# Kernel optimization log

Hardware: AMD Instinct MI355X
Metric: run time of the kernel (lower is better)

The kernel has to match this reference:

```python
import jax, jax.numpy as jnp
import numpy as np

CODEBOOK_BITS = 8      # log2(256)
NUM_Q = 2              # NUM_QUANTIZERS
INV_TEMP = 100.0       # LFQ default inv_temperature
DIVERSITY_GAMMA = 1.0
ENTROPY_WEIGHT = 0.1   # LFQ default entropy_loss_weight
COMMIT_WEIGHT = 1.0


def conv2d(x, w, b, pad):
    out = jax.lax.conv_general_dilated(
        x, w, (1, 1), [(pad, pad), (pad, pad)],
        dimension_numbers=('NCHW', 'OIHW', 'NCHW'))
    return out + b[None, :, None, None]


def maxpool2(x):
    return jax.lax.reduce_window(x, -jnp.inf, jax.lax.max,
                                 (1, 1, 2, 2), (1, 1, 2, 2), 'VALID')


def groupnorm(x, groups=4, eps=1e-5):
    B, C, H, W = x.shape
    xg = x.reshape(B, groups, C // groups, H, W)
    mu = xg.mean(axis=(2, 3, 4), keepdims=True)
    var = xg.var(axis=(2, 3, 4), keepdims=True)
    return ((xg - mu) * jax.lax.rsqrt(var + eps)).reshape(B, C, H, W)


def upsample2(x):  # nearest, scale 2
    return jnp.repeat(jnp.repeat(x, 2, axis=2), 2, axis=3)


def lfq_codebook():
    # all 2^8 sign patterns, code j has bit i = ((j>>i)&1)*2-1
    j = jnp.arange(2 ** CODEBOOK_BITS)
    bits = ((j[:, None] >> jnp.arange(CODEBOOK_BITS)[None, :]) & 1).astype(jnp.float32)
    return bits * 2.0 - 1.0  # [256, 8]


def lfq_residual(z):
    # z: (B, D, H, W) with D = CODEBOOK_BITS
    codebook = lfq_codebook()
    t = jnp.transpose(z, (0, 2, 3, 1))  # (B,H,W,D) tokens
    residual = t
    quantized_out = jnp.zeros_like(t)
    pow2 = (2 ** jnp.arange(CODEBOOK_BITS)).astype(jnp.int32)
    indices = []
    aux = jnp.zeros((), t.dtype)
    for _ in range(NUM_Q):
        q_hard = jnp.where(residual > 0, 1.0, -1.0).astype(t.dtype)
        # straight-through binarization
        q = residual + jax.lax.stop_gradient(q_hard - residual)
        idx = jnp.sum((q_hard > 0).astype(jnp.int32) * pow2, axis=-1)  # (B,H,W)
        logits = (2.0 * INV_TEMP) * jnp.einsum('bhwd,cd->bhwc', residual, codebook)
        logp = jax.nn.log_softmax(logits, axis=-1)
        probs = jnp.exp(logp)
        per_sample_entropy = -jnp.mean(jnp.sum(probs * logp, axis=-1))
        avg_prob = jnp.mean(probs.reshape(-1, probs.shape[-1]), axis=0)
        codebook_entropy = -jnp.sum(avg_prob * jnp.log(avg_prob + 1e-10))
        entropy_aux = per_sample_entropy - DIVERSITY_GAMMA * codebook_entropy
        commit = jnp.mean((residual - jax.lax.stop_gradient(q_hard)) ** 2)
        aux = aux + ENTROPY_WEIGHT * entropy_aux + COMMIT_WEIGHT * commit
        quantized_out = quantized_out + q
        residual = residual - jax.lax.stop_gradient(q)
        indices.append(idx)
    q_out = jnp.transpose(quantized_out, (0, 3, 1, 2))  # (B,D,H,W)
    return q_out, jnp.stack(indices, axis=-1), aux


def setup_inputs() -> dict:
    key = jax.random.key(0)
    ks = jax.random.split(key, 13)
    s = 0.05
    return {
        'x': jax.random.normal(ks[0], (32, 1, 256, 256), jnp.float32),
        'w1': jax.random.normal(ks[1], (16, 1, 3, 3), jnp.float32) * s,
        'b1': jax.random.normal(ks[2], (16,), jnp.float32) * s,
        'w2': jax.random.normal(ks[3], (32, 16, 3, 3), jnp.float32) * s,
        'b2': jax.random.normal(ks[4], (32,), jnp.float32) * s,
        'w3': jax.random.normal(ks[5], (8, 32, 1, 1), jnp.float32) * s,
        'b3': jax.random.normal(ks[6], (8,), jnp.float32) * s,
        'd1': jax.random.normal(ks[7], (32, 8, 3, 3), jnp.float32) * s,
        'db1': jax.random.normal(ks[8], (32,), jnp.float32) * s,
        'd2': jax.random.normal(ks[9], (16, 32, 3, 3), jnp.float32) * s,
        'db2': jax.random.normal(ks[10], (16,), jnp.float32) * s,
        'd3': jax.random.normal(ks[11], (1, 16, 3, 3), jnp.float32) * s,
        'db3': jax.random.normal(ks[12], (1,), jnp.float32) * s,
    }


def reference(x, w1, b1, w2, b2, w3, b3, d1, db1, d2, db2, d3, db3):
    # encode
    h = jax.nn.gelu(maxpool2(conv2d(x, w1, b1, pad=1)), approximate=False)
    h = groupnorm(maxpool2(conv2d(h, w2, b2, pad=1)))
    h = conv2d(h, w3, b3, pad=0)  # (B,8,64,64)
    # residual LFQ
    q, indices, aux = lfq_residual(h)
    # decode
    y = upsample2(conv2d(q, d1, db1, pad=1))
    y = upsample2(jax.nn.gelu(conv2d(y, d2, db2, pad=1), approximate=False))
    y = conv2d(y, d3, db3, pad=1)
    return jnp.clip(y, -1.0, 1.0), indices, aux
```

## Files before the change

kernel.cpp:

```cpp
#include <hip/hip_runtime.h>
#include <hip/hip_bf16.h>
#include <math.h>

#define DEV __device__ __forceinline__

DEV float gelu_exact(float x){ return 0.5f*x*(1.0f + erff(x*0.70710678118654752f)); }

__global__ __launch_bounds__(256) void k_prep(const float* __restrict__ w2,
    const float* __restrict__ d2, float* __restrict__ w2t, float* __restrict__ wp4d2)
{
  const int gid = blockIdx.x*256 + threadIdx.x;
  for(int i=gid;i<4608;i+=2048){
    int oc=i/144, rem=i-oc*144, ic=rem/9, k=rem-ic*9;
    w2t[(ic*32+oc)*9+k]=w2[i];
  }
  for(int i=gid;i<2048;i+=2048){
    int par=i>>9, ic=(i>>4)&31, oc=i&15;
    int py=par>>1, px=par&1;
    const float* wg = d2 + ((size_t)oc*32+ic)*9;
    float a00=0.f,a01=0.f,a10=0.f,a11=0.f;
    #pragma unroll
    for(int ky=0;ky<3;ky++){
      int sy = py ? (ky>>1) : ((ky>0)?1:0);
      #pragma unroll
      for(int kx=0;kx<3;kx++){
        int sx = px ? (kx>>1) : ((kx>0)?1:0);
        float wv=wg[ky*3+kx];
        if(sy==0){ if(sx==0)a00+=wv; else a01+=wv; }
        else     { if(sx==0)a10+=wv; else a11+=wv; }
      }
    }
    float* dst=wp4d2+(size_t)i*4;
    dst[0]=a00; dst[1]=a01; dst[2]=a10; dst[3]=a11;
  }
}

__global__ __launch_bounds__(256) void k_conv1(const float* __restrict__ x,
    const float* __restrict__ w1, const float* __restrict__ b1,
    float* __restrict__ h1)
{
  __shared__ float sE[34*19], sO[34*19];
  const int b = blockIdx.z;
  const int r0 = blockIdx.x*32, c0 = blockIdx.y*32;
  const float* xp = x + (size_t)b*65536;
  for(int i=threadIdx.x;i<34*34;i+=256){
    int r=i/34, c=i-r*34;
    int gr=r0+r-1, gc=c0+c-1;
    float v=0.f;
    if(gr>=0 && gr<256 && gc>=0 && gc<256) v = xp[gr*256+gc];
    if(c&1) sO[r*19+(c>>1)]=v; else sE[r*19+(c>>1)]=v;
  }
  __syncthreads();
  const int tx=threadIdx.x&15, ty=threadIdx.x>>4;
  const int base = 2*ty*19 + tx;
  float in[4][4];
  #pragma unroll
  for(int r=0;r<4;r++){
    in[r][0]=sE[base+r*19]; in[r][1]=sO[base+r*19];
    in[r][2]=sE[base+r*19+1]; in[r][3]=sO[base+r*19+1];
  }
  const int py = blockIdx.x*16+ty, px = blockIdx.y*16+tx;
  float* op = h1 + ((size_t)b*16)*16384 + py*128 + px;
  #pragma unroll
  for(int ch=0;ch<16;ch++){
    float m=-1e30f;
    #pragma unroll
    for(int pr=0;pr<2;pr++)
      #pragma unroll
      for(int pc=0;pc<2;pc++){
        float a=0.f;
        #pragma unroll
        for(int ky=0;ky<3;ky++)
          #pragma unroll
          for(int kx=0;kx<3;kx++)
            a = fmaf(in[pr+ky][pc+kx], w1[ch*9+ky*3+kx], a);
        m = fmaxf(m,a);
      }
    op[(size_t)ch*16384] = gelu_exact(m + b1[ch]);
  }
}

__global__ __launch_bounds__(256) void k_conv2(const float* __restrict__ h1,
    const float* __restrict__ w2t, const float* __restrict__ b2,
    float* __restrict__ h2, double* __restrict__ pb)
{
  __shared__ __align__(16) float t2[8*360];
  const int b=blockIdx.z;
  const int r0=blockIdx.x*16, c0=blockIdx.y*16;
  const float* hp = h1 + (size_t)b*16*16384;
  const int pos=threadIdx.x&63;
  const int ocg=__builtin_amdgcn_readfirstlane((int)(threadIdx.x>>6));
  const int oc0=ocg*8;
  const int pyl=pos>>3, pxl=pos&7;
  const int base0 = 2*pyl*20 + 2*pxl;
  float acc[8][4];
  #pragma unroll
  for(int o=0;o<8;o++)
    #pragma unroll
    for(int j=0;j<4;j++) acc[o][j]=0.f;

  for(int half=0;half<2;half++){
    for(int i=threadIdx.x;i<1296;i+=256){
      int ic=i/162, rem=i-ic*162, lr=rem/9, jp=rem-lr*9;
      int gr=r0+lr-1, gc=c0+2*jp-1;
      float v0=0.f, v1=0.f;
      if(gr>=0&&gr<128){
        const float* row=hp+(size_t)(half*8+ic)*16384+(size_t)gr*128;
        if(gc>=0&&gc<128) v0=row[gc];
        if(gc+1<128)      v1=row[gc+1];
      }
      *(float2*)&t2[ic*360+lr*20+2*jp]=make_float2(v0,v1);
    }
    __syncthreads();
    #pragma unroll 4
    for(int ic=0;ic<8;ic++){
      float in[4][4];
      #pragma unroll
      for(int r=0;r<4;r++){
        float2 a=*(const float2*)&t2[ic*360 + base0 + r*20];
        float2 c=*(const float2*)&t2[ic*360 + base0 + r*20 + 2];
        in[r][0]=a.x; in[r][1]=a.y; in[r][2]=c.x; in[r][3]=c.y;
      }
      const float* wp = w2t + ((half*8+ic)*32+oc0)*9;
      #pragma unroll
      for(int o=0;o<8;o++){
        #pragma unroll
        for(int pr=0;pr<2;pr++)
          #pragma unroll
          for(int pc=0;pc<2;pc++){
            float s=acc[o][pr*2+pc];
            #pragma unroll
            for(int ky=0;ky<3;ky++)
              #pragma unroll
              for(int kx=0;kx<3;kx++)
                s=fmaf(in[pr+ky][pc+kx], wp[o*9+ky*3+kx], s);
            acc[o][pr*2+pc]=s;
          }
      }
    }
    __syncthreads();
  }
  const int py=blockIdx.x*8+pyl, px=blockIdx.y*8+pxl;
  double s=0.0, s2=0.0;
  #pragma unroll
  for(int o=0;o<8;o++){
    const int oc=oc0+o;
    float m=fmaxf(fmaxf(acc[o][0],acc[o][1]),fmaxf(acc[o][2],acc[o][3]));
    float hv=m+b2[oc];
    h2[(((size_t)b*32+oc)*64+py)*64+px]=hv;
    s += (double)hv; s2 += (double)hv*(double)hv;
  }
  #pragma unroll
  for(int off=32;off;off>>=1){
    s  += __shfl_xor(s,  off, 64);
    s2 += __shfl_xor(s2, off, 64);
  }
  if(pos==0){
    const int bidx = blockIdx.x*8 + blockIdx.y;
    double* p = pb + (((size_t)b*4+ocg)*64 + bidx)*2;
    p[0]=s; p[1]=s2;
  }
}

__global__ __launch_bounds__(64) void k_stats2(const double* __restrict__ pb,
                                               float* __restrict__ stats)
{
  const int bg=blockIdx.x, t=threadIdx.x;
  double s = pb[((size_t)bg*64+t)*2], s2 = pb[((size_t)bg*64+t)*2+1];
  #pragma unroll
  for(int off=32;off;off>>=1){
    s  += __shfl_xor(s,  off, 64);
    s2 += __shfl_xor(s2, off, 64);
  }
  if(t==0){
    double mu=s/32768.0;
    double var=s2/32768.0 - mu*mu;
    stats[bg]=(float)mu;
    stats[128+bg]=(float)(1.0/sqrt(var+1e-5));
  }
}

__global__ __launch_bounds__(256) void k_lfq(const float* __restrict__ h2,
    const float* __restrict__ stats, const float* __restrict__ w3, const float* __restrict__ b3,
    float* __restrict__ qout, float* __restrict__ idxout,
    float* __restrict__ avgp, float* __restrict__ ec)
{
  __shared__ __align__(16) float tabL[16*258];
  __shared__ __align__(16) float tabH[16*258];
  const int blk=blockIdx.x;
  const int b=blk>>4;
  const int t=threadIdx.x;
  const int h=(blk&15)*4 + (t>>6);
  const int w=t&63;
  float mu[4], rs[4];
  #pragma unroll
  for(int g=0;g<4;g++){ mu[g]=stats[b*4+g]; rs[g]=stats[128+b*4+g]; }
  const float* hp = h2 + (size_t)b*131072 + h*64 + w;
  float z[8];
  #pragma unroll
  for(int d=0;d<8;d++) z[d]=b3[d];
  #pragma unroll
  for(int c=0;c<32;c++){
    float xn=(hp[(size_t)c*4096]-mu[c>>3])*rs[c>>3];
    #pragma unroll
    for(int d=0;d<8;d++) z[d]=fmaf(xn, w3[d*32+c], z[d]);
  }
  float r[8], qsum[8];
  #pragma unroll
  for(int d=0;d<8;d++){ r[d]=z[d]; qsum[d]=0.f; }
  float entk[2], comk[2];
  #pragma unroll
  for(int k=0;k<2;k++){
    int idx=0; float ent=0.f, com=0.f;
    float pb0[8], pb1[8];
    #pragma unroll
    for(int d=0;d<8;d++){
      float rv=r[d];
      bool pos = rv>0.f;
      float sgn = pos?1.f:-1.f;
      idx |= (pos?1:0)<<d;
      float dd=rv-sgn; com=fmaf(dd,dd,com);
      float a=400.f*fabsf(rv);
      float e=__expf(-a);
      float p=1.f/(1.f+e);
      ent += a - p*a - __logf(p);
      float pm=p, pq=1.f-p;
      pb1[d]=pos?pm:pq;
      pb0[d]=pos?pq:pm;
      qsum[d]+=sgn;
      r[d]=rv-sgn;
    }
    float lo[16], hi[16];
    lo[0]=pb0[0]; lo[1]=pb1[0];
    lo[2]=lo[0]*pb1[1]; lo[3]=lo[1]*pb1[1]; lo[0]*=pb0[1]; lo[1]*=pb0[1];
    lo[4]=lo[0]*pb1[2]; lo[5]=lo[1]*pb1[2]; lo[6]=lo[2]*pb1[2]; lo[7]=lo[3]*pb1[2];
    lo[0]*=pb0[2]; lo[1]*=pb0[2]; lo[2]*=pb0[2]; lo[3]*=pb0[2];
    lo[8]=lo[0]*pb1[3]; lo[9]=lo[1]*pb1[3]; lo[10]=lo[2]*pb1[3]; lo[11]=lo[3]*pb1[3];
    lo[12]=lo[4]*pb1[3]; lo[13]=lo[5]*pb1[3]; lo[14]=lo[6]*pb1[3]; lo[15]=lo[7]*pb1[3];
    lo[0]*=pb0[3]; lo[1]*=pb0[3]; lo[2]*=pb0[3]; lo[3]*=pb0[3];
    lo[4]*=pb0[3]; lo[5]*=pb0[3]; lo[6]*=pb0[3]; lo[7]*=pb0[3];
    hi[0]=pb0[4]; hi[1]=pb1[4];
    hi[2]=hi[0]*pb1[5]; hi[3]=hi[1]*pb1[5]; hi[0]*=pb0[5]; hi[1]*=pb0[5];
    hi[4]=hi[0]*pb1[6]; hi[5]=hi[1]*pb1[6]; hi[6]=hi[2]*pb1[6]; hi[7]=hi[3]*pb1[6];
    hi[0]*=pb0[6]; hi[1]*=pb0[6]; hi[2]*=pb0[6]; hi[3]*=pb0[6];
    hi[8]=hi[0]*pb1[7]; hi[9]=hi[1]*pb1[7]; hi[10]=hi[2]*pb1[7]; hi[11]=hi[3]*pb1[7];
    hi[12]=hi[4]*pb1[7]; hi[13]=hi[5]*pb1[7]; hi[14]=hi[6]*pb1[7]; hi[15]=hi[7]*pb1[7];
    hi[0]*=pb0[7]; hi[1]*=pb0[7]; hi[2]*=pb0[7]; hi[3]*=pb0[7];
    hi[4]*=pb0[7]; hi[5]*=pb0[7]; hi[6]*=pb0[7]; hi[7]*=pb0[7];
    #pragma unroll
    for(int m=0;m<16;m++){ tabL[m*258+t]=lo[m]; tabH[m*258+t]=hi[m]; }
    __syncthreads();
    float accp=0.f, accq=0.f;
    const int jl=t&15, jh=t>>4;
    const float* Lp=&tabL[jl*258];
    const float* Hp=&tabH[jh*258];
    #pragma unroll 8
    for(int q=0;q<128;q++){
      float2 L=*(const float2*)&Lp[2*q];
      float2 H=*(const float2*)&Hp[2*q];
      accp=fmaf(L.x,H.x,accp); accq=fmaf(L.y,H.y,accq);
    }
    avgp[((size_t)k*512+blk)*256+t]=accp+accq;
    __syncthreads();
    entk[k]=ent; comk[k]=com;
    idxout[((size_t)(b*64+h)*64+w)*2+k]=(float)idx;
  }
  #pragma unroll
  for(int d=0;d<8;d++)
    qout[(((size_t)b*8+d)*64+h)*64+w]=qsum[d];
  tabL[t]=entk[0]; tabL[256+t]=entk[1]; tabL[512+t]=comk[0]; tabL[768+t]=comk[1];
  __syncthreads();
  for(int st=128;st>0;st>>=1){
    if(t<st){ tabL[t]+=tabL[t+st]; tabL[256+t]+=tabL[256+t+st];
              tabL[512+t]+=tabL[512+t+st]; tabL[768+t]+=tabL[768+t+st]; }
    __syncthreads();
  }
  if(t==0){ ec[blk*4+0]=tabL[0]; ec[blk*4+1]=tabL[256]; ec[blk*4+2]=tabL[512]; ec[blk*4+3]=tabL[768]; }
}

__global__ __launch_bounds__(256) void k_red(const float* __restrict__ avgp,
    float* __restrict__ avgs)
{
  const int k=blockIdx.x>>4, c0=(blockIdx.x&15)*16;
  const int col=threadIdx.x&15, rg=threadIdx.x>>4;
  float s=0.f;
  for(int j=0;j<32;j++){
    int blk=rg+16*j;
    s+=avgp[((size_t)k*512+blk)*256+c0+col];
  }
  __shared__ float red[256];
  red[threadIdx.x]=s; __syncthreads();
  for(int st=128;st>=16;st>>=1){
    if(threadIdx.x<st) red[threadIdx.x]+=red[threadIdx.x+st];
    __syncthreads();
  }
  if(threadIdx.x<16) avgs[k*256+c0+threadIdx.x]=red[threadIdx.x];
}

__global__ __launch_bounds__(256) void k_final(const float* __restrict__ avgs,
    const float* __restrict__ ec, float* __restrict__ auxout)
{
  __shared__ double red[256];
  const int t=threadIdx.x;
  double cb=0.0;
  #pragma unroll
  for(int k=0;k<2;k++){
    double ap=(double)avgs[k*256+t]*(1.0/131072.0);
    cb += -(ap*log(ap+1e-10));
  }
  red[t]=cb; __syncthreads();
  for(int st=128;st>0;st>>=1){ if(t<st) red[t]+=red[t+st]; __syncthreads(); }
  double CB=red[0]; __syncthreads();
  double e=0.0,c=0.0;
  for(int blk=t;blk<512;blk+=256){
    e += (double)ec[blk*4+0]+(double)ec[blk*4+1];
    c += (double)ec[blk*4+2]+(double)ec[blk*4+3];
  }
  red[t]=e; __syncthreads();
  for(int st=128;st>0;st>>=1){ if(t<st) red[t]+=red[t+st]; __syncthreads(); }
  double E=red[0]; __syncthreads();
  red[t]=c; __syncthreads();
  for(int st=128;st>0;st>>=1){ if(t<st) red[t]+=red[t+st]; __syncthreads(); }
  if(t==0){
    double C=red[0];
    double aux = 0.1*(E*(1.0/131072.0) - CB) + C*(1.0/1048576.0);
    auxout[0]=(float)aux;
  }
}

__global__ __launch_bounds__(256) void k_dec1(const float* __restrict__ q,
    const float* __restrict__ d1, const float* __restrict__ db1, float* __restrict__ out1)
{
  __shared__ float tile[8*110];
  const int b=blockIdx.z, r0=blockIdx.x*8, c0=blockIdx.y*8;
  const float* qp = q + (size_t)b*8*4096;
  for(int i=threadIdx.x;i<800;i+=256){
    int ic=i/100, rem=i-ic*100, r=rem/10, c=rem-r*10;
    int gr=r0+r-1, gc=c0+c-1;
    float v=0.f;
    if(gr>=0&&gr<64&&gc>=0&&gc<64) v=qp[ic*4096+gr*64+gc];
    tile[ic*110+r*11+c]=v;
  }
  __syncthreads();
  const int ocg=__builtin_amdgcn_readfirstlane((int)(threadIdx.x>>6));
  const int oc0=ocg*8;
  const int l=threadIdx.x&63, ry=l>>3, cx=l&7;
  float acc[8];
  #pragma unroll
  for(int o=0;o<8;o++) acc[o]=db1[oc0+o];
  #pragma unroll 2
  for(int ic=0;ic<8;ic++){
    float v[9];
    #pragma unroll
    for(int ky=0;ky<3;ky++)
      #pragma unroll
      for(int kx=0;kx<3;kx++)
        v[ky*3+kx]=tile[ic*110+(ry+ky)*11+cx+kx];
    #pragma unroll
    for(int o=0;o<8;o++){
      const float* wp=&d1[((oc0+o)*8+ic)*9];
      float s=acc[o];
      #pragma unroll
      for(int kk=0;kk<9;kk++) s=fmaf(v[kk],wp[kk],s);
      acc[o]=s;
    }
  }
  #pragma unroll
  for(int o=0;o<8;o++)
    out1[(((size_t)b*32+oc0+o)*64 + r0+ry)*64 + c0+cx]=acc[o];
}

__global__ __launch_bounds__(256) void k_dec2(const float* __restrict__ out1,
    const float* __restrict__ wp4d2, const float* __restrict__ db2, float* __restrict__ out2)
{
  __shared__ float tile[32*110];
  const int b=blockIdx.z, y0=blockIdx.x*16, x0=blockIdx.y*16;
  const int sy0=(y0>>1)-1, sx0=(x0>>1)-1;
  const float* sp = out1 + (size_t)b*32*4096;
  for(int i=threadIdx.x;i<3200;i+=256){
    int ic=i/100, rem=i-ic*100, r=rem/10, c=rem-r*10;
    int gr=sy0+r, gc=sx0+c;
    float v=0.f;
    if(gr>=0&&gr<64&&gc>=0&&gc<64) v=sp[ic*4096+gr*64+gc];
    tile[ic*110+r*11+c]=v;
  }
  __syncthreads();
  const int par=__builtin_amdgcn_readfirstlane((int)(threadIdx.x>>6));
  const int py=par>>1, px=par&1;
  const int l=threadIdx.x&63, ry=l>>3, cx=l&7;
  const int byl=ry+py, bxl=cx+px;
  float acc[16];
  #pragma unroll
  for(int o=0;o<16;o++) acc[o]=db2[o];
  #pragma unroll 2
  for(int ic=0;ic<32;ic++){
    const float* tp=&tile[ic*110 + byl*11 + bxl];
    const float s00=tp[0], s01=tp[1], s10=tp[11], s11=tp[12];
    const float* wq = wp4d2 + (size_t)((par*32+ic)*16)*4;
    #pragma unroll
    for(int o=0;o<16;o++)
      acc[o]=fmaf(s00,wq[o*4],fmaf(s01,wq[o*4+1],fmaf(s10,wq[o*4+2],fmaf(s11,wq[o*4+3],acc[o]))));
  }
  const int Y=y0+2*ry+py, X=x0+2*cx+px;
  #pragma unroll
  for(int o=0;o<16;o++)
    out2[((size_t)b*16+o)*16384 + (size_t)Y*128 + X] = gelu_exact(acc[o]);
}

__global__ __launch_bounds__(256) void k_dec3(const float* __restrict__ out2,
    const float* __restrict__ d3, const float* __restrict__ db3, float* __restrict__ y)
{
  __shared__ float tile[16*342];
  __shared__ float4 wp4[64];
  const int b=blockIdx.z, y0=blockIdx.x*32, x0=blockIdx.y*32;
  const int sy0=(y0>>1)-1, sx0=(x0>>1)-1;
  const float* sp = out2 + (size_t)b*16*16384;
  for(int i=threadIdx.x;i<16*324;i+=256){
    int ic=i/324, rem=i-ic*324, r=rem/18, c=rem-r*18;
    int gr=sy0+r, gc=sx0+c;
    float v=0.f;
    if(gr>=0&&gr<128&&gc>=0&&gc<128) v=sp[ic*16384+gr*128+gc];
    tile[ic*342+r*19+c]=v;
  }
  if(threadIdx.x<64){
    int par=threadIdx.x>>4, ic=threadIdx.x&15;
    int py=par>>1, px=par&1;
    const float* wg = d3 + ic*9;
    float a00=0.f,a01=0.f,a10=0.f,a11=0.f;
    #pragma unroll
    for(int ky=0;ky<3;ky++){
      int sy = py ? (ky>>1) : ((ky>0)?1:0);
      #pragma unroll
      for(int kx=0;kx<3;kx++){
        int sx = px ? (kx>>1) : ((kx>0)?1:0);
        float wv=wg[ky*3+kx];
        if(sy==0){ if(sx==0)a00+=wv; else a01+=wv; }
        else     { if(sx==0)a10+=wv; else a11+=wv; }
      }
    }
    wp4[threadIdx.x]=make_float4(a00,a01,a10,a11);
  }
  __syncthreads();
  const float bias=db3[0];
  const int par=__builtin_amdgcn_readfirstlane((int)(threadIdx.x>>6));
  const int py=par>>1, px=par&1;
  const int l=threadIdx.x&63, r0l=l>>4, cl=l&15;
  const int bxl=cl+px;
  float acc[4];
  #pragma unroll
  for(int a=0;a<4;a++) acc[a]=bias;
  #pragma unroll 2
  for(int ic=0;ic<16;ic++){
    const float4 wv=wp4[par*16+ic];
    #pragma unroll
    for(int a=0;a<4;a++){
      const int byl=r0l+4*a+py;
      const float* tp=&tile[ic*342 + byl*19 + bxl];
      acc[a]=fmaf(tp[0],wv.x,fmaf(tp[1],wv.y,fmaf(tp[19],wv.z,fmaf(tp[20],wv.w,acc[a]))));
    }
  }
  #pragma unroll
  for(int a=0;a<4;a++){
    const int yy=2*(r0l+4*a)+py, xx=2*cl+px;
    float v=fminf(fmaxf(acc[a],-1.0f),1.0f);
    y[(size_t)b*65536 + (size_t)(y0+yy)*256 + (x0+xx)] = v;
  }
}

extern "C" void kernel_launch(void* const* d_in, const int* in_sizes, int n_in,
                              void* d_out, int out_size, void* d_ws, size_t ws_size,
                              hipStream_t stream)
{
  const float* x  =(const float*)d_in[0];
  const float* w1 =(const float*)d_in[1];
  const float* b1 =(const float*)d_in[2];
  const float* w2 =(const float*)d_in[3];
  const float* b2 =(const float*)d_in[4];
  const float* w3 =(const float*)d_in[5];
  const float* b3 =(const float*)d_in[6];
  const float* d1 =(const float*)d_in[7];
  const float* db1=(const float*)d_in[8];
  const float* d2 =(const float*)d_in[9];
  const float* db2=(const float*)d_in[10];
  const float* d3 =(const float*)d_in[11];
  const float* db3=(const float*)d_in[12];
  float* out=(float*)d_out;
  float* ws =(float*)d_ws;
  float* h1   = ws;
  float* h2   = ws + 8388608;
  float* qb   = ws + 12582912;
  float* st   = ws + 13631488;
  float* avgp = ws + 13631744;
  float* ec   = ws + 13893888;
  float* w2t  = avgp;
  float* wp4d2= ws + 13895936;
  float* avgs = ws + 13904128;
  double* pb  = (double*)qb;
  float* out1 = h2;
  float* out2 = h1;

  k_prep  <<<dim3(8),256,0,stream>>>(w2,d2,w2t,wp4d2);
  k_conv1 <<<dim3(8,8,32),256,0,stream>>>(x,w1,b1,h1);
  k_conv2 <<<dim3(8,8,32),256,0,stream>>>(h1,w2t,b2,h2,pb);
  k_stats2<<<dim3(128),64,0,stream>>>(pb,st);
  k_lfq   <<<dim3(512),256,0,stream>>>(h2,st,w3,b3,qb,out+2097152,avgp,ec);
  k_red   <<<dim3(32),256,0,stream>>>(avgp,avgs);
  k_final <<<dim3(1),256,0,stream>>>(avgs,ec,out+2359296);
  k_dec1  <<<dim3(8,8,32),256,0,stream>>>(qb,d1,db1,out1);
  k_dec2  <<<dim3(8,8,32),256,0,stream>>>(out1,wp4d2,db2,out2);
  k_dec3  <<<dim3(8,8,32),256,0,stream>>>(out2,d3,db3,out);
}
```

Measured before the change: 202.3 us.

## Fold weight prep into conv1, prefetch second channel half in conv2, widen LFQ loads

The separate weight-preparation kernel is removed and its work moved into eight conv1 blocks, saving one launch. In conv2 both halves of the input channels are loaded into registers up front and staged into a double-buffered shared tile, so the second half's global loads overlap the first half's compute and one barrier is dropped. The LFQ probability tables are padded to a stride of 260 and read as float4 instead of float2, halving the number of shared-memory loads. The trade-off is higher register and shared-memory use in conv2, which may lower occupancy.

After: 192.2 us. 5.0% less time.

```diff
diff --git a/kernel.cpp b/kernel.cpp
--- a/kernel.cpp
+++ b/kernel.cpp
@@ -6,38 +6,11 @@
 
 DEV float gelu_exact(float x){ return 0.5f*x*(1.0f + erff(x*0.70710678118654752f)); }
 
-__global__ __launch_bounds__(256) void k_prep(const float* __restrict__ w2,
-    const float* __restrict__ d2, float* __restrict__ w2t, float* __restrict__ wp4d2)
-{
-  const int gid = blockIdx.x*256 + threadIdx.x;
-  for(int i=gid;i<4608;i+=2048){
-    int oc=i/144, rem=i-oc*144, ic=rem/9, k=rem-ic*9;
-    w2t[(ic*32+oc)*9+k]=w2[i];
-  }
-  for(int i=gid;i<2048;i+=2048){
-    int par=i>>9, ic=(i>>4)&31, oc=i&15;
-    int py=par>>1, px=par&1;
-    const float* wg = d2 + ((size_t)oc*32+ic)*9;
-    float a00=0.f,a01=0.f,a10=0.f,a11=0.f;
-    #pragma unroll
-    for(int ky=0;ky<3;ky++){
-      int sy = py ? (ky>>1) : ((ky>0)?1:0);
-      #pragma unroll
-      for(int kx=0;kx<3;kx++){
-        int sx = px ? (kx>>1) : ((kx>0)?1:0);
-        float wv=wg[ky*3+kx];
-        if(sy==0){ if(sx==0)a00+=wv; else a01+=wv; }
-        else     { if(sx==0)a10+=wv; else a11+=wv; }
-      }
-    }
-    float* dst=wp4d2+(size_t)i*4;
-    dst[0]=a00; dst[1]=a01; dst[2]=a10; dst[3]=a11;
-  }
-}
-
 __global__ __launch_bounds__(256) void k_conv1(const float* __restrict__ x,
     const float* __restrict__ w1, const float* __restrict__ b1,
-    float* __restrict__ h1)
+    float* __restrict__ h1,
+    const float* __restrict__ w2, const float* __restrict__ d2,
+    float* __restrict__ w2t, float* __restrict__ wp4d2)
 {
   __shared__ float sE[34*19], sO[34*19];
   const int b = blockIdx.z;
@@ -78,18 +51,78 @@
       }
     op[(size_t)ch*16384] = gelu_exact(m + b1[ch]);
   }
+  if(blockIdx.x==0 && blockIdx.y==0 && b<8){
+    const int gid = b*256 + threadIdx.x;
+    for(int i=gid;i<4608;i+=2048){
+      int oc=i/144, rem=i-oc*144, ic=rem/9, k=rem-ic*9;
+      w2t[(ic*32+oc)*9+k]=w2[i];
+    }
+    for(int i=gid;i<2048;i+=2048){
+      int par=i>>9, ic=(i>>4)&31, oc=i&15;
+      int pyp=par>>1, pxp=par&1;
+      const float* wg = d2 + ((size_t)oc*32+ic)*9;
+      float a00=0.f,a01=0.f,a10=0.f,a11=0.f;
+      #pragma unroll
+      for(int ky=0;ky<3;ky++){
+        int sy = pyp ? (ky>>1) : ((ky>0)?1:0);
+        #pragma unroll
+        for(int kx=0;kx<3;kx++){
+          int sx = pxp ? (kx>>1) : ((kx>0)?1:0);
+          float wv=wg[ky*3+kx];
+          if(sy==0){ if(sx==0)a00+=wv; else a01+=wv; }
+          else     { if(sx==0)a10+=wv; else a11+=wv; }
+        }
+      }
+      float* dst=wp4d2+(size_t)i*4;
+      dst[0]=a00; dst[1]=a01; dst[2]=a10; dst[3]=a11;
+    }
+  }
 }
 
 __global__ __launch_bounds__(256) void k_conv2(const float* __restrict__ h1,
     const float* __restrict__ w2t, const float* __restrict__ b2,
     float* __restrict__ h2, double* __restrict__ pb)
 {
-  __shared__ __align__(16) float t2[8*360];
+  __shared__ __align__(16) float t2[2][8*360];
   const int b=blockIdx.z;
   const int r0=blockIdx.x*16, c0=blockIdx.y*16;
   const float* hp = h1 + (size_t)b*16*16384;
-  const int pos=threadIdx.x&63;
-  const int ocg=__builtin_amdgcn_readfirstlane((int)(threadIdx.x>>6));
+  const int t=threadIdx.x;
+  int lofs[6]; int gof[6]; bool ok0[6], ok1[6];
+  #pragma unroll
+  for(int s=0;s<6;s++){
+    int idx=s*256+t;
+    int ic=idx/162, rem=idx-162*ic, lr=rem/9, jp=rem-9*lr;
+    int gr=r0+lr-1, gc=c0+2*jp-1;
+    bool rok = (gr>=0) && (gr<128);
+    ok0[s] = rok && (gc>=0);
+    ok1[s] = rok && (gc+1<128);
+    lofs[s]= ic*360+lr*20+2*jp;
+    gof[s] = ic*16384 + gr*128 + gc;
+  }
+  float a0[6], a1[6], c0r[6], c1r[6];
+  #pragma unroll
+  for(int s=0;s<6;s++){
+    if(s<5 || t<16){
+      a0[s] = ok0[s] ? hp[gof[s]]   : 0.f;
+      a1[s] = ok1[s] ? hp[gof[s]+1] : 0.f;
+    }
+  }
+  #pragma unroll
+  for(int s=0;s<6;s++)
+    if(s<5 || t<16) *(float2*)&t2[0][lofs[s]]=make_float2(a0[s],a1[s]);
+  const float* hp1 = hp + 8*16384;
+  #pragma unroll
+  for(int s=0;s<6;s++){
+    if(s<5 || t<16){
+      c0r[s] = ok0[s] ? hp1[gof[s]]   : 0.f;
+      c1r[s] = ok1[s] ? hp1[gof[s]+1] : 0.f;
+    }
+  }
+  __syncthreads();
+
+  const int pos=t&63;
+  const int ocg=__builtin_amdgcn_readfirstlane((int)(t>>6));
   const int oc0=ocg*8;
   const int pyl=pos>>3, pxl=pos&7;
   const int base0 = 2*pyl*20 + 2*pxl;
@@ -99,47 +132,63 @@
     #pragma unroll
     for(int j=0;j<4;j++) acc[o][j]=0.f;
 
-  for(int half=0;half<2;half++){
-    for(int i=threadIdx.x;i<1296;i+=256){
-      int ic=i/162, rem=i-ic*162, lr=rem/9, jp=rem-lr*9;
-      int gr=r0+lr-1, gc=c0+2*jp-1;
-      float v0=0.f, v1=0.f;
-      if(gr>=0&&gr<128){
-        const float* row=hp+(size_t)(half*8+ic)*16384+(size_t)gr*128;
-        if(gc>=0&&gc<128) v0=row[gc];
-        if(gc+1<128)      v1=row[gc+1];
-      }
-      *(float2*)&t2[ic*360+lr*20+2*jp]=make_float2(v0,v1);
-    }
-    __syncthreads();
-    #pragma unroll 4
-    for(int ic=0;ic<8;ic++){
-      float in[4][4];
-      #pragma unroll
-      for(int r=0;r<4;r++){
-        float2 a=*(const float2*)&t2[ic*360 + base0 + r*20];
-        float2 c=*(const float2*)&t2[ic*360 + base0 + r*20 + 2];
-        in[r][0]=a.x; in[r][1]=a.y; in[r][2]=c.x; in[r][3]=c.y;
-      }
-      const float* wp = w2t + ((half*8+ic)*32+oc0)*9;
-      #pragma unroll
-      for(int o=0;o<8;o++){
+  #pragma unroll 4
+  for(int ic=0;ic<8;ic++){
+    float in[4][4];
+    #pragma unroll
+    for(int r=0;r<4;r++){
+      float2 a=*(const float2*)&t2[0][ic*360 + base0 + r*20];
+      float2 c=*(const float2*)&t2[0][ic*360 + base0 + r*20 + 2];
+      in[r][0]=a.x; in[r][1]=a.y; in[r][2]=c.x; in[r][3]=c.y;
+    }
+    const float* wp = w2t + (ic*32+oc0)*9;
+    #pragma unroll
+    for(int o=0;o<8;o++){
+      #pragma unroll
+      for(int pr=0;pr<2;pr++)
         #pragma unroll
-        for(int pr=0;pr<2;pr++)
+        for(int pc=0;pc<2;pc++){
+          float s=acc[o][pr*2+pc];
           #pragma unroll
-          for(int pc=0;pc<2;pc++){
-            float s=acc[o][pr*2+pc];
+          for(int ky=0;ky<3;ky++)
             #pragma unroll
-            for(int ky=0;ky<3;ky++)
-              #pragma unroll
-              for(int kx=0;kx<3;kx++)
-                s=fmaf(in[pr+ky][pc+kx], wp[o*9+ky*3+kx], s);
-            acc[o][pr*2+pc]=s;
-          }
-      }
-    }
-    __syncthreads();
-  }
+            for(int kx=0;kx<3;kx++)
+              s=fmaf(in[pr+ky][pc+kx], wp[o*9+ky*3+kx], s);
+          acc[o][pr*2+pc]=s;
+        }
+    }
+  }
+  #pragma unroll
+  for(int s=0;s<6;s++)
+    if(s<5 || t<16) *(float2*)&t2[1][lofs[s]]=make_float2(c0r[s],c1r[s]);
+  __syncthreads();
+  #pragma unroll 4
+  for(int ic=0;ic<8;ic++){
+    float in[4][4];
+    #pragma unroll
+    for(int r=0;r<4;r++){
+      float2 a=*(const float2*)&t2[1][ic*360 + base0 + r*20];
+      float2 c=*(const float2*)&t2[1][ic*360 + base0 + r*20 + 2];
+      in[r][0]=a.x; in[r][1]=a.y; in[r][2]=c.x; in[r][3]=c.y;
+    }
+    const float* wp = w2t + ((8+ic)*32+oc0)*9;
+    #pragma unroll
+    for(int o=0;o<8;o++){
+      #pragma unroll
+      for(int pr=0;pr<2;pr++)
+        #pragma unroll
+        for(int pc=0;pc<2;pc++){
+          float s=acc[o][pr*2+pc];
+          #pragma unroll
+          for(int ky=0;ky<3;ky++)
+            #pragma unroll
+            for(int kx=0;kx<3;kx++)
+              s=fmaf(in[pr+ky][pc+kx], wp[o*9+ky*3+kx], s);
+          acc[o][pr*2+pc]=s;
+        }
+    }
+  }
+
   const int py=blockIdx.x*8+pyl, px=blockIdx.y*8+pxl;
   double s=0.0, s2=0.0;
   #pragma unroll
@@ -185,8 +234,8 @@
     float* __restrict__ qout, float* __restrict__ idxout,
     float* __restrict__ avgp, float* __restrict__ ec)
 {
-  __shared__ __align__(16) float tabL[16*258];
-  __shared__ __align__(16) float tabH[16*258];
+  __shared__ __align__(16) float tabL[16*260];
+  __shared__ __align__(16) float tabH[16*260];
   const int blk=blockIdx.x;
   const int b=blk>>4;
   const int t=threadIdx.x;
@@ -248,17 +297,18 @@
     hi[0]*=pb0[7]; hi[1]*=pb0[7]; hi[2]*=pb0[7]; hi[3]*=pb0[7];
     hi[4]*=pb0[7]; hi[5]*=pb0[7]; hi[6]*=pb0[7]; hi[7]*=pb0[7];
     #pragma unroll
-    for(int m=0;m<16;m++){ tabL[m*258+t]=lo[m]; tabH[m*258+t]=hi[m]; }
+    for(int m=0;m<16;m++){ tabL[m*260+t]=lo[m]; tabH[m*260+t]=hi[m]; }
     __syncthreads();
     float accp=0.f, accq=0.f;
     const int jl=t&15, jh=t>>4;
-    const float* Lp=&tabL[jl*258];
-    const float* Hp=&tabH[jh*258];
-    #pragma unroll 8
-    for(int q=0;q<128;q++){
-      float2 L=*(const float2*)&Lp[2*q];
-      float2 H=*(const float2*)&Hp[2*q];
+    const float* Lp=&tabL[jl*260];
+    const float* Hp=&tabH[jh*260];
+    #pragma unroll 4
+    for(int q4=0;q4<64;q4++){
+      float4 L=*(const float4*)&Lp[4*q4];
+      float4 H=*(const float4*)&Hp[4*q4];
       accp=fmaf(L.x,H.x,accp); accq=fmaf(L.y,H.y,accq);
+      accp=fmaf(L.z,H.z,accp); accq=fmaf(L.w,H.w,accq);
     }
     avgp[((size_t)k*512+blk)*256+t]=accp+accq;
     __syncthreads();
@@ -499,8 +549,7 @@
   float* out1 = h2;
   float* out2 = h1;
 
-  k_prep  <<<dim3(8),256,0,stream>>>(w2,d2,w2t,wp4d2);
-  k_conv1 <<<dim3(8,8,32),256,0,stream>>>(x,w1,b1,h1);
+  k_conv1 <<<dim3(8,8,32),256,0,stream>>>(x,w1,b1,h1,w2,d2,w2t,wp4d2);
   k_conv2 <<<dim3(8,8,32),256,0,stream>>>(h1,w2t,b2,h2,pb);
   k_stats2<<<dim3(128),64,0,stream>>>(pb,st);
   k_lfq   <<<dim3(512),256,0,stream>>>(h2,st,w3,b3,qb,out+2097152,avgp,ec);
```
